# Kernel optimization log

Measured on AMD Instinct MI355X. Metric: run time of the kernel, lower is better.

Reference implementation:

```python
import jax, jax.numpy as jnp
import numpy as np


def setup_inputs() -> dict:
    key = jax.random.key(0)
    B, C, T = 16, 128, 8192
    x = jax.random.normal(key, (B, C, T), dtype=jnp.float32)
    return {"x": x}


def reference(x) -> jnp.ndarray:
    # x: (B, C, T) real EEG signals
    B, C, T = x.shape
    # "Analytic" signal as in the torch code: zero FFT bins >= T//2, then ifft.
    Xf = jnp.fft.fft(x, axis=-1)                       # complex64 (B, C, T)
    keep = (jnp.arange(T) < (T // 2))                  # (T,)
    Xf = jnp.where(keep, Xf, 0.0 + 0.0j)
    xa = jnp.fft.ifft(Xf, axis=-1)                     # complex analytic signal
    phase = jnp.arctan2(xa.imag, xa.real)              # == torch.angle, (B, C, T)

    # PLV_ij = |mean_t exp(i(phase_i - phase_j))|
    # Decompose: Re = mean(cos_i cos_j + sin_i sin_j), Im = mean(sin_i cos_j - cos_i sin_j)
    cos_p = jnp.cos(phase)                             # (B, C, T)
    sin_p = jnp.sin(phase)
    inv_t = jnp.float32(1.0 / T)
    re = (jnp.einsum('bct,bdt->bcd', cos_p, cos_p)
          + jnp.einsum('bct,bdt->bcd', sin_p, sin_p)) * inv_t
    im = (jnp.einsum('bct,bdt->bcd', sin_p, cos_p)
          - jnp.einsum('bct,bdt->bcd', cos_p, sin_p)) * inv_t
    plv = jnp.sqrt(re * re + im * im)                  # (B, C, C)
    return plv
```

## Files before the change

### kernel.cpp

```cpp
#include <hip/hip_runtime.h>
#include <hip/hip_fp16.h>
#include <math.h>

#define T_LEN 8192
#define CHN 128
#define BATCH 16
#define NKCHUNK 16

typedef short bf16x8 __attribute__((ext_vector_type(8)));
typedef float f32x16 __attribute__((ext_vector_type(16)));

#define SIN8 0.3826834323650898f
#define COS8 0.9238795325112868f
#define SROW 72
#define SPLANE (128 * SROW)

__device__ __forceinline__ ushort f2bf(float f) {
    unsigned u = __float_as_uint(f);
    unsigned r = (u + 0x7fffu + ((u >> 16) & 1u)) >> 16;
    return (ushort)r;
}

__device__ __forceinline__ void barrier_lds_only() {
    asm volatile("s_waitcnt lgkmcnt(0)" ::: "memory");
    __builtin_amdgcn_s_barrier();
}

__device__ __forceinline__ float2 cadd(float2 a, float2 b) { return make_float2(a.x + b.x, a.y + b.y); }
__device__ __forceinline__ float2 csub(float2 a, float2 b) { return make_float2(a.x - b.x, a.y - b.y); }
__device__ __forceinline__ float2 cmul(float2 a, float2 b) {
    return make_float2(a.x * b.x - a.y * b.y, a.x * b.y + a.y * b.x);
}

__device__ __forceinline__ void r4f(float2 x0, float2 x1, float2 x2, float2 x3,
                                    float2 wa, float2 wb, float2 wc,
                                    float2& y0, float2& y1, float2& y2, float2& y3) {
    float2 t0 = cadd(x0, x2), t1 = csub(x0, x2);
    float2 t2 = cadd(x1, x3), t3 = csub(x1, x3);
    y0 = cadd(t0, t2);
    y1 = cmul(csub(t0, t2), wb);
    y2 = cmul(make_float2(t1.x + t3.y, t1.y - t3.x), wa);
    y3 = cmul(make_float2(t1.x - t3.y, t1.y + t3.x), wc);
}

__device__ __forceinline__ void r4i(float2 x0, float2 x1, float2 x2, float2 x3,
                                    float2 wa, float2 wb, float2 wc,
                                    float2& y0, float2& y1, float2& y2, float2& y3) {
    float2 a1 = cmul(x1, wb);
    float2 a2 = cmul(x2, wa);
    float2 a3 = cmul(x3, wc);
    float2 u0 = cadd(x0, a1), u1 = csub(x0, a1);
    float2 p = cadd(a2, a3);
    float2 m = make_float2(-(a2.y - a3.y), a2.x - a3.x);
    y0 = cadd(u0, p); y2 = csub(u0, p);
    y1 = cadd(u1, m); y3 = csub(u1, m);
}

__device__ __forceinline__ void r8f(const float2* x, float sn, float cs, float2* y) {
    const float r22 = 0.70710678118654752f;
    float2 w1 = make_float2(cs, sn);
    float2 w2 = make_float2(cs * cs - sn * sn, 2.f * cs * sn);
    float2 w4 = cmul(w2, w2);
    float2 w6 = cmul(w4, w2);
    float2 u0 = cadd(x[0], x[4]), u1 = cadd(x[1], x[5]), u2 = cadd(x[2], x[6]), u3 = cadd(x[3], x[7]);
    float2 e0 = cmul(csub(x[0], x[4]), w1);
    float2 e1 = cmul(csub(x[1], x[5]), w1);
    float2 e2 = cmul(csub(x[2], x[6]), w1);
    float2 e3 = cmul(csub(x[3], x[7]), w1);
    float2 v0 = e0;
    float2 v1 = make_float2(r22 * (e1.x + e1.y), r22 * (e1.y - e1.x));
    float2 v2 = make_float2(e2.y, -e2.x);
    float2 v3 = make_float2(r22 * (e3.y - e3.x), -r22 * (e3.x + e3.y));
    r4f(u0, u1, u2, u3, w2, w4, w6, y[0], y[1], y[2], y[3]);
    r4f(v0, v1, v2, v3, w2, w4, w6, y[4], y[5], y[6], y[7]);
}

__device__ __forceinline__ void r8i(const float2* x, float sn, float cs, float2* y) {
    const float r22 = 0.70710678118654752f;
    float2 w1 = make_float2(cs, sn);
    float2 w2 = make_float2(cs * cs - sn * sn, 2.f * cs * sn);
    float2 w4 = cmul(w2, w2);
    float2 w6 = cmul(w4, w2);
    float2 g0, g1, g2, g3, g4, g5, g6, g7;
    r4i(x[0], x[1], x[2], x[3], w2, w4, w6, g0, g1, g2, g3);
    r4i(x[4], x[5], x[6], x[7], w2, w4, w6, g4, g5, g6, g7);
    float2 t0 = cmul(g4, w1);
    float2 e1 = cmul(g5, w1);
    float2 e2 = cmul(g6, w1);
    float2 e3 = cmul(g7, w1);
    float2 t1 = make_float2(r22 * (e1.x - e1.y), r22 * (e1.x + e1.y));
    float2 t2 = make_float2(-e2.y, e2.x);
    float2 t3 = make_float2(-r22 * (e3.x + e3.y), r22 * (e3.x - e3.y));
    y[0] = cadd(g0, t0); y[4] = csub(g0, t0);
    y[1] = cadd(g1, t1); y[5] = csub(g1, t1);
    y[2] = cadd(g2, t2); y[6] = csub(g2, t2);
    y[3] = cadd(g3, t3); y[7] = csub(g3, t3);
}

__global__ __launch_bounds__(512, 4) void fft_analytic_kernel(const float* __restrict__ x,
                                                              ushort* __restrict__ zc,
                                                              ushort* __restrict__ zs) {
    __shared__ __align__(16) float2 buf[T_LEN];
    const int tid = threadIdx.x;
    const int row = blockIdx.x;
    const float* xr = x + ((size_t)row << 13);

    for (int s = 0; s < 2; ++s) {
        const int g = tid + (s << 9);
        float2 X[8], Y[8];
#pragma unroll
        for (int c = 0; c < 8; ++c) X[c] = make_float2(xr[g + (c << 10)], 0.f);
        float sn, cs;
        __sincosf(-(float)M_PI / 4096.f * (float)g, &sn, &cs);
        r8f(X, sn, cs, Y);
#pragma unroll
        for (int c = 0; c < 8; ++c) buf[g + (c << 10)] = Y[c];
    }
    __syncthreads();

    {
        const float astep = -(float)M_PI / 512.f;
        for (int s = 0; s < 2; ++s) {
            const int g = tid + (s << 9);
            const int j = g & 127;
            const int i = ((g & ~127) << 3) | j;
            float2 xx[8], yy[8];
#pragma unroll
            for (int c = 0; c < 8; ++c) xx[c] = buf[i + c * 128];
            float sn, cs;
            __sincosf(astep * (float)j, &sn, &cs);
            r8f(xx, sn, cs, yy);
#pragma unroll
            for (int c = 0; c < 8; ++c) buf[i + c * 128] = yy[c];
        }
        __syncthreads();
    }

    {
        const float astep = -(float)M_PI / 64.f;
        for (int s = 0; s < 2; ++s) {
            const int g = tid + (s << 9);
            const int j = g & 15;
            const int i = ((g & ~15) << 3) | j;
            float2 xx[8], yy[8];
#pragma unroll
            for (int c = 0; c < 8; ++c) xx[c] = buf[i + c * 16];
            float sn, cs;
            __sincosf(astep * (float)j, &sn, &cs);
            r8f(xx, sn, cs, yy);
#pragma unroll
            for (int c = 0; c < 8; ++c) buf[(i + c * 16) ^ (2 * c)] = yy[c];
        }
        __syncthreads();
    }

    {
        float2 v[16];
        float4* bb = (float4*)buf;
        const int K = tid & 7;
#pragma unroll
        for (int p = 0; p < 8; ++p) {
            float4 f = bb[8 * tid + (p ^ K)];
            v[2 * p]     = make_float2(f.x, f.y);
            v[2 * p + 1] = make_float2(f.z, f.w);
        }
        float2 xe[8], xo[8], E[8], O[8], t[8];
#pragma unroll
        for (int c = 0; c < 8; ++c) { xe[c] = v[2 * c]; xo[c] = v[2 * c + 1]; }
        r8f(xe, 0.f, 1.f, E);
        r8f(xo, -SIN8, COS8, O);
#pragma unroll
        for (int c = 0; c < 8; ++c) t[c] = cadd(E[c], O[c]);
        r8i(t, 0.f, 1.f, xe);
        r8i(t, SIN8, COS8, xo);
#pragma unroll
        for (int p = 0; p < 8; ++p)
            bb[8 * tid + (p ^ K)] = make_float4(xe[p].x, xe[p].y, xo[p].x, xo[p].y);
    }
    __syncthreads();

    {
        const float astep = (float)M_PI / 64.f;
        for (int s = 0; s < 2; ++s) {
            const int g = tid + (s << 9);
            const int j = g & 15;
            const int i = ((g & ~15) << 3) | j;
            float2 xx[8], yy[8];
#pragma unroll
            for (int c = 0; c < 8; ++c) xx[c] = buf[(i + c * 16) ^ (2 * c)];
            float sn, cs;
            __sincosf(astep * (float)j, &sn, &cs);
            r8i(xx, sn, cs, yy);
#pragma unroll
            for (int c = 0; c < 8; ++c) buf[i + c * 16] = yy[c];
        }
        __syncthreads();
    }

    {
        const float astep = (float)M_PI / 512.f;
        for (int s = 0; s < 2; ++s) {
            const int g = tid + (s << 9);
            const int j = g & 127;
            const int i = ((g & ~127) << 3) | j;
            float2 xx[8], yy[8];
#pragma unroll
            for (int c = 0; c < 8; ++c) xx[c] = buf[i + c * 128];
            float sn, cs;
            __sincosf(astep * (float)j, &sn, &cs);
            r8i(xx, sn, cs, yy);
#pragma unroll
            for (int c = 0; c < 8; ++c) buf[i + c * 128] = yy[c];
        }
        __syncthreads();
    }

    ushort* zcr = zc + ((size_t)row << 13);
    ushort* zsr = zs + ((size_t)row << 13);
    for (int s = 0; s < 2; ++s) {
        const int g = tid + (s << 9);
        float2 xx[8], yy[8];
#pragma unroll
        for (int c = 0; c < 8; ++c) xx[c] = buf[g + (c << 10)];
        float sn, cs;
        __sincosf((float)M_PI / 4096.f * (float)g, &sn, &cs);
        r8i(xx, sn, cs, yy);
#pragma unroll
        for (int c = 0; c < 8; ++c) {
            float2 vv = yy[c];
            float n2 = vv.x * vv.x + vv.y * vv.y;
            float cc = 1.f, ss = 0.f;
            if (n2 > 0.f) { float inv = rsqrtf(n2); cc = vv.x * inv; ss = vv.y * inv; }
            zcr[g + (c << 10)] = f2bf(cc);
            zsr[g + (c << 10)] = f2bf(ss);
        }
    }
}

__global__ __launch_bounds__(512, 2) void gram_kernel(const ushort* __restrict__ zc,
                                                      const ushort* __restrict__ zs,
                                                      __half2* __restrict__ partial) {
    const int b = blockIdx.x, kc = blockIdx.y;
    const int tid = threadIdx.x;
    const int wave = tid >> 6;
    const int wr = wave & 3, wcol = wave >> 2;
    const int lane31 = tid & 31;
    const int half = (tid >> 5) & 1;

    __shared__ __align__(16) ushort sZ[2 * SPLANE];

    f32x16 accRe[2], accIm[2];
#pragma unroll
    for (int v = 0; v < 2; ++v)
#pragma unroll
        for (int r = 0; r < 16; ++r) { accRe[v][r] = 0.f; accIm[v][r] = 0.f; }

    const size_t base = ((size_t)b * CHN) << 13;
    const int k0 = kc << 9;

    const ushort* srcs[4];
    int ldst[4];
#pragma unroll
    for (int q = 0; q < 4; ++q) {
        int id = tid + (q << 9);
        int plane = id >> 10;
        int rid = (id >> 3) & 127;
        int ck = id & 7;
        srcs[q] = (plane ? zs : zc) + base + ((size_t)rid << 13) + (size_t)(k0 + ck * 8);
        ldst[q] = plane * SPLANE + rid * SROW + ck * 8;
    }

    uint4 pre[2][4];
#pragma unroll
    for (int q = 0; q < 4; ++q) pre[0][q] = *(const uint4*)srcs[q];
#pragma unroll
    for (int q = 0; q < 4; ++q) pre[1][q] = *(const uint4*)(srcs[q] + 64);

#pragma unroll
    for (int it = 0; it < 8; ++it) {
        barrier_lds_only();
#pragma unroll
        for (int q = 0; q < 4; ++q) *(uint4*)&sZ[ldst[q]] = pre[it & 1][q];
        if (it < 6) {
#pragma unroll
            for (int q = 0; q < 4; ++q)
                pre[it & 1][q] = *(const uint4*)(srcs[q] + (it + 2) * 64);
        }
        barrier_lds_only();
#pragma unroll
        for (int kb = 0; kb < 64; kb += 16) {
            const int aoff = (wr * 32 + lane31) * SROW + kb + half * 8;
            bf16x8 aC = *(const bf16x8*)&sZ[aoff];
            bf16x8 aS = *(const bf16x8*)&sZ[SPLANE + aoff];
            bf16x8 aCn;
#pragma unroll
            for (int r = 0; r < 8; ++r) aCn[r] = (short)(aC[r] ^ (short)0x8000);
            bf16x8 bC[2], bS[2];
#pragma unroll
            for (int v = 0; v < 2; ++v) {
                const int boff = (wcol * 64 + v * 32 + lane31) * SROW + kb + half * 8;
                bC[v] = *(const bf16x8*)&sZ[boff];
                bS[v] = *(const bf16x8*)&sZ[SPLANE + boff];
            }
            accRe[0] = __builtin_amdgcn_mfma_f32_32x32x16_bf16(aC,  bC[0], accRe[0], 0, 0, 0);
            accRe[1] = __builtin_amdgcn_mfma_f32_32x32x16_bf16(aC,  bC[1], accRe[1], 0, 0, 0);
            accIm[0] = __builtin_amdgcn_mfma_f32_32x32x16_bf16(aS,  bC[0], accIm[0], 0, 0, 0);
            accIm[1] = __builtin_amdgcn_mfma_f32_32x32x16_bf16(aS,  bC[1], accIm[1], 0, 0, 0);
            accRe[0] = __builtin_amdgcn_mfma_f32_32x32x16_bf16(aS,  bS[0], accRe[0], 0, 0, 0);
            accRe[1] = __builtin_amdgcn_mfma_f32_32x32x16_bf16(aS,  bS[1], accRe[1], 0, 0, 0);
            accIm[0] = __builtin_amdgcn_mfma_f32_32x32x16_bf16(aCn, bS[0], accIm[0], 0, 0, 0);
            accIm[1] = __builtin_amdgcn_mfma_f32_32x32x16_bf16(aCn, bS[1], accIm[1], 0, 0, 0);
        }
    }

    __half2* pb = partial + ((size_t)(kc * BATCH + b) << 14);
#pragma unroll
    for (int v = 0; v < 2; ++v)
#pragma unroll
        for (int r = 0; r < 16; ++r) {
            int rrow = (r & 3) + 8 * (r >> 2) + 4 * half;
            int i = wr * 32 + rrow;
            int j = wcol * 64 + v * 32 + lane31;
            pb[i * CHN + j] = __floats2half2_rn(accRe[v][r], accIm[v][r]);
        }
}

__global__ __launch_bounds__(256) void reduce_kernel(const __half2* __restrict__ partial,
                                                     float* __restrict__ out) {
    const size_t i = (size_t)blockIdx.x * 256 + threadIdx.x;
    const size_t n = (size_t)BATCH * CHN * CHN;
    if (i >= n) return;
    float re = 0.0f, im = 0.0f;
#pragma unroll
    for (int c = 0; c < NKCHUNK; ++c) {
        float2 p = __half22float2(partial[(size_t)c * n + i]);
        re += p.x;
        im += p.y;
    }
    out[i] = sqrtf(re * re + im * im) * (1.0f / (float)T_LEN);
}

extern "C" void kernel_launch(void* const* d_in, const int* in_sizes, int n_in,
                              void* d_out, int out_size, void* d_ws, size_t ws_size,
                              hipStream_t stream) {
    const float* x = (const float*)d_in[0];
    float* out = (float*)d_out;

    const size_t plane_elems = (size_t)BATCH * CHN * T_LEN;
    ushort* zc = (ushort*)d_ws;
    ushort* zs = zc + plane_elems;
    __half2* partial = (__half2*)((char*)d_ws + 2 * plane_elems * sizeof(ushort));

    fft_analytic_kernel<<<BATCH * CHN, 512, 0, stream>>>(x, zc, zs);

    dim3 g2(BATCH, NKCHUNK);
    gram_kernel<<<g2, 512, 0, stream>>>(zc, zs, partial);

    const int n_out = BATCH * CHN * CHN;
    reduce_kernel<<<(n_out + 255) / 256, 256, 0, stream>>>(partial, out);
}
```

Measured before the change: 177.4 us.

## Precompute FFT twiddles once per thread and split gram kernel across column halves

The FFT kernel now computes each stage's twiddle set once with hardware sin/cos in revolution units and reuses it for the matching inverse stages through conjugate multiplies, instead of calling sincos in every stage. The gram kernel grid gains a column-half dimension, so each block computes a 128x64 tile with one accumulator pair per wave, doubling the number of blocks. This is meant to cut transcendental work and raise occupancy and parallelism in the gram step. The cost is that every block reloads its full A and B slices, so global and LDS traffic rises, and the held twiddles use more registers.

```diff
diff --git a/kernel.cpp b/kernel.cpp
--- a/kernel.cpp
+++ b/kernel.cpp
@@ -12,6 +12,7 @@
 
 #define SIN8 0.3826834323650898f
 #define COS8 0.9238795325112868f
+#define R22  0.70710678118654752f
 #define SROW 72
 #define SPLANE (128 * SROW)
 
@@ -30,6 +31,22 @@
 __device__ __forceinline__ float2 csub(float2 a, float2 b) { return make_float2(a.x - b.x, a.y - b.y); }
 __device__ __forceinline__ float2 cmul(float2 a, float2 b) {
     return make_float2(a.x * b.x - a.y * b.y, a.x * b.y + a.y * b.x);
+}
+__device__ __forceinline__ float2 cmulc(float2 a, float2 b) {
+    return make_float2(a.x * b.x + a.y * b.y, a.y * b.x - a.x * b.y);
+}
+
+struct W8 { float2 w1, w2, w4, w6; };
+
+__device__ __forceinline__ W8 mkw(float rev) {
+    W8 w;
+    float sn = __builtin_amdgcn_sinf(rev);
+    float cs = __builtin_amdgcn_cosf(rev);
+    w.w1 = make_float2(cs, sn);
+    w.w2 = make_float2(cs * cs - sn * sn, 2.f * cs * sn);
+    w.w4 = cmul(w.w2, w.w2);
+    w.w6 = cmul(w.w4, w.w2);
+    return w;
 }
 
 __device__ __forceinline__ void r4f(float2 x0, float2 x1, float2 x2, float2 x3,
@@ -43,12 +60,12 @@
     y3 = cmul(make_float2(t1.x - t3.y, t1.y + t3.x), wc);
 }
 
-__device__ __forceinline__ void r4i(float2 x0, float2 x1, float2 x2, float2 x3,
-                                    float2 wa, float2 wb, float2 wc,
-                                    float2& y0, float2& y1, float2& y2, float2& y3) {
-    float2 a1 = cmul(x1, wb);
-    float2 a2 = cmul(x2, wa);
-    float2 a3 = cmul(x3, wc);
+__device__ __forceinline__ void r4i_c(float2 x0, float2 x1, float2 x2, float2 x3,
+                                      float2 wa, float2 wb, float2 wc,
+                                      float2& y0, float2& y1, float2& y2, float2& y3) {
+    float2 a1 = cmulc(x1, wb);
+    float2 a2 = cmulc(x2, wa);
+    float2 a3 = cmulc(x3, wc);
     float2 u0 = cadd(x0, a1), u1 = csub(x0, a1);
     float2 p = cadd(a2, a3);
     float2 m = make_float2(-(a2.y - a3.y), a2.x - a3.x);
@@ -56,41 +73,31 @@
     y1 = cadd(u1, m); y3 = csub(u1, m);
 }
 
-__device__ __forceinline__ void r8f(const float2* x, float sn, float cs, float2* y) {
-    const float r22 = 0.70710678118654752f;
-    float2 w1 = make_float2(cs, sn);
-    float2 w2 = make_float2(cs * cs - sn * sn, 2.f * cs * sn);
-    float2 w4 = cmul(w2, w2);
-    float2 w6 = cmul(w4, w2);
+__device__ __forceinline__ void r8f_w(const float2* x, W8 w, float2* y) {
     float2 u0 = cadd(x[0], x[4]), u1 = cadd(x[1], x[5]), u2 = cadd(x[2], x[6]), u3 = cadd(x[3], x[7]);
-    float2 e0 = cmul(csub(x[0], x[4]), w1);
-    float2 e1 = cmul(csub(x[1], x[5]), w1);
-    float2 e2 = cmul(csub(x[2], x[6]), w1);
-    float2 e3 = cmul(csub(x[3], x[7]), w1);
+    float2 e0 = cmul(csub(x[0], x[4]), w.w1);
+    float2 e1 = cmul(csub(x[1], x[5]), w.w1);
+    float2 e2 = cmul(csub(x[2], x[6]), w.w1);
+    float2 e3 = cmul(csub(x[3], x[7]), w.w1);
     float2 v0 = e0;
-    float2 v1 = make_float2(r22 * (e1.x + e1.y), r22 * (e1.y - e1.x));
+    float2 v1 = make_float2(R22 * (e1.x + e1.y), R22 * (e1.y - e1.x));
     float2 v2 = make_float2(e2.y, -e2.x);
-    float2 v3 = make_float2(r22 * (e3.y - e3.x), -r22 * (e3.x + e3.y));
-    r4f(u0, u1, u2, u3, w2, w4, w6, y[0], y[1], y[2], y[3]);
-    r4f(v0, v1, v2, v3, w2, w4, w6, y[4], y[5], y[6], y[7]);
-}
-
-__device__ __forceinline__ void r8i(const float2* x, float sn, float cs, float2* y) {
-    const float r22 = 0.70710678118654752f;
-    float2 w1 = make_float2(cs, sn);
-    float2 w2 = make_float2(cs * cs - sn * sn, 2.f * cs * sn);
-    float2 w4 = cmul(w2, w2);
-    float2 w6 = cmul(w4, w2);
+    float2 v3 = make_float2(R22 * (e3.y - e3.x), -R22 * (e3.x + e3.y));
+    r4f(u0, u1, u2, u3, w.w2, w.w4, w.w6, y[0], y[1], y[2], y[3]);
+    r4f(v0, v1, v2, v3, w.w2, w.w4, w.w6, y[4], y[5], y[6], y[7]);
+}
+
+__device__ __forceinline__ void r8i_w(const float2* x, W8 w, float2* y) {
     float2 g0, g1, g2, g3, g4, g5, g6, g7;
-    r4i(x[0], x[1], x[2], x[3], w2, w4, w6, g0, g1, g2, g3);
-    r4i(x[4], x[5], x[6], x[7], w2, w4, w6, g4, g5, g6, g7);
-    float2 t0 = cmul(g4, w1);
-    float2 e1 = cmul(g5, w1);
-    float2 e2 = cmul(g6, w1);
-    float2 e3 = cmul(g7, w1);
-    float2 t1 = make_float2(r22 * (e1.x - e1.y), r22 * (e1.x + e1.y));
+    r4i_c(x[0], x[1], x[2], x[3], w.w2, w.w4, w.w6, g0, g1, g2, g3);
+    r4i_c(x[4], x[5], x[6], x[7], w.w2, w.w4, w.w6, g4, g5, g6, g7);
+    float2 t0 = cmulc(g4, w.w1);
+    float2 e1 = cmulc(g5, w.w1);
+    float2 e2 = cmulc(g6, w.w1);
+    float2 e3 = cmulc(g7, w.w1);
+    float2 t1 = make_float2(R22 * (e1.x - e1.y), R22 * (e1.x + e1.y));
     float2 t2 = make_float2(-e2.y, e2.x);
-    float2 t3 = make_float2(-r22 * (e3.x + e3.y), r22 * (e3.x - e3.y));
+    float2 t3 = make_float2(-R22 * (e3.x + e3.y), R22 * (e3.x - e3.y));
     y[0] = cadd(g0, t0); y[4] = csub(g0, t0);
     y[1] = cadd(g1, t1); y[5] = csub(g1, t1);
     y[2] = cadd(g2, t2); y[6] = csub(g2, t2);
@@ -105,56 +112,54 @@
     const int row = blockIdx.x;
     const float* xr = x + ((size_t)row << 13);
 
+    W8 wL[2];
+    const W8 w128 = mkw((float)(tid & 127) * (-1.f / 1024.f));
+    const W8 w16  = mkw((float)(tid & 15)  * (-1.f / 128.f));
+
+#pragma unroll
     for (int s = 0; s < 2; ++s) {
         const int g = tid + (s << 9);
         float2 X[8], Y[8];
 #pragma unroll
         for (int c = 0; c < 8; ++c) X[c] = make_float2(xr[g + (c << 10)], 0.f);
-        float sn, cs;
-        __sincosf(-(float)M_PI / 4096.f * (float)g, &sn, &cs);
-        r8f(X, sn, cs, Y);
+        wL[s] = mkw((float)g * (-1.f / 8192.f));
+        r8f_w(X, wL[s], Y);
 #pragma unroll
         for (int c = 0; c < 8; ++c) buf[g + (c << 10)] = Y[c];
     }
     __syncthreads();
 
+#pragma unroll
+    for (int s = 0; s < 2; ++s) {
+        const int g = tid + (s << 9);
+        const int i = ((g & ~127) << 3) | (g & 127);
+        float2 xx[8], yy[8];
+#pragma unroll
+        for (int c = 0; c < 8; ++c) xx[c] = buf[i + c * 128];
+        r8f_w(xx, w128, yy);
+#pragma unroll
+        for (int c = 0; c < 8; ++c) buf[i + c * 128] = yy[c];
+    }
+    __syncthreads();
+
+#pragma unroll
+    for (int s = 0; s < 2; ++s) {
+        const int g = tid + (s << 9);
+        const int i = ((g & ~15) << 3) | (g & 15);
+        float2 xx[8], yy[8];
+#pragma unroll
+        for (int c = 0; c < 8; ++c) xx[c] = buf[i + c * 16];
+        r8f_w(xx, w16, yy);
+#pragma unroll
+        for (int c = 0; c < 8; ++c) buf[(i + c * 16) ^ (2 * c)] = yy[c];
+    }
+    __syncthreads();
+
     {
-        const float astep = -(float)M_PI / 512.f;
-        for (int s = 0; s < 2; ++s) {
-            const int g = tid + (s << 9);
-            const int j = g & 127;
-            const int i = ((g & ~127) << 3) | j;
-            float2 xx[8], yy[8];
-#pragma unroll
-            for (int c = 0; c < 8; ++c) xx[c] = buf[i + c * 128];
-            float sn, cs;
-            __sincosf(astep * (float)j, &sn, &cs);
-            r8f(xx, sn, cs, yy);
-#pragma unroll
-            for (int c = 0; c < 8; ++c) buf[i + c * 128] = yy[c];
-        }
-        __syncthreads();
-    }
-
-    {
-        const float astep = -(float)M_PI / 64.f;
-        for (int s = 0; s < 2; ++s) {
-            const int g = tid + (s << 9);
-            const int j = g & 15;
-            const int i = ((g & ~15) << 3) | j;
-            float2 xx[8], yy[8];
-#pragma unroll
-            for (int c = 0; c < 8; ++c) xx[c] = buf[i + c * 16];
-            float sn, cs;
-            __sincosf(astep * (float)j, &sn, &cs);
-            r8f(xx, sn, cs, yy);
-#pragma unroll
-            for (int c = 0; c < 8; ++c) buf[(i + c * 16) ^ (2 * c)] = yy[c];
-        }
-        __syncthreads();
-    }
-
-    {
+        const W8 wID = { make_float2(1.f, 0.f), make_float2(1.f, 0.f),
+                         make_float2(1.f, 0.f), make_float2(1.f, 0.f) };
+        const W8 wO  = { make_float2(COS8, -SIN8), make_float2(R22, -R22),
+                         make_float2(0.f, -1.f),   make_float2(-R22, -R22) };
         float2 v[16];
         float4* bb = (float4*)buf;
         const int K = tid & 7;
@@ -167,64 +172,53 @@
         float2 xe[8], xo[8], E[8], O[8], t[8];
 #pragma unroll
         for (int c = 0; c < 8; ++c) { xe[c] = v[2 * c]; xo[c] = v[2 * c + 1]; }
-        r8f(xe, 0.f, 1.f, E);
-        r8f(xo, -SIN8, COS8, O);
+        r8f_w(xe, wID, E);
+        r8f_w(xo, wO, O);
 #pragma unroll
         for (int c = 0; c < 8; ++c) t[c] = cadd(E[c], O[c]);
-        r8i(t, 0.f, 1.f, xe);
-        r8i(t, SIN8, COS8, xo);
+        r8i_w(t, wID, xe);
+        r8i_w(t, wO, xo);
 #pragma unroll
         for (int p = 0; p < 8; ++p)
             bb[8 * tid + (p ^ K)] = make_float4(xe[p].x, xe[p].y, xo[p].x, xo[p].y);
     }
     __syncthreads();
 
-    {
-        const float astep = (float)M_PI / 64.f;
-        for (int s = 0; s < 2; ++s) {
-            const int g = tid + (s << 9);
-            const int j = g & 15;
-            const int i = ((g & ~15) << 3) | j;
-            float2 xx[8], yy[8];
-#pragma unroll
-            for (int c = 0; c < 8; ++c) xx[c] = buf[(i + c * 16) ^ (2 * c)];
-            float sn, cs;
-            __sincosf(astep * (float)j, &sn, &cs);
-            r8i(xx, sn, cs, yy);
-#pragma unroll
-            for (int c = 0; c < 8; ++c) buf[i + c * 16] = yy[c];
-        }
-        __syncthreads();
-    }
-
-    {
-        const float astep = (float)M_PI / 512.f;
-        for (int s = 0; s < 2; ++s) {
-            const int g = tid + (s << 9);
-            const int j = g & 127;
-            const int i = ((g & ~127) << 3) | j;
-            float2 xx[8], yy[8];
-#pragma unroll
-            for (int c = 0; c < 8; ++c) xx[c] = buf[i + c * 128];
-            float sn, cs;
-            __sincosf(astep * (float)j, &sn, &cs);
-            r8i(xx, sn, cs, yy);
-#pragma unroll
-            for (int c = 0; c < 8; ++c) buf[i + c * 128] = yy[c];
-        }
-        __syncthreads();
-    }
+#pragma unroll
+    for (int s = 0; s < 2; ++s) {
+        const int g = tid + (s << 9);
+        const int i = ((g & ~15) << 3) | (g & 15);
+        float2 xx[8], yy[8];
+#pragma unroll
+        for (int c = 0; c < 8; ++c) xx[c] = buf[(i + c * 16) ^ (2 * c)];
+        r8i_w(xx, w16, yy);
+#pragma unroll
+        for (int c = 0; c < 8; ++c) buf[i + c * 16] = yy[c];
+    }
+    __syncthreads();
+
+#pragma unroll
+    for (int s = 0; s < 2; ++s) {
+        const int g = tid + (s << 9);
+        const int i = ((g & ~127) << 3) | (g & 127);
+        float2 xx[8], yy[8];
+#pragma unroll
+        for (int c = 0; c < 8; ++c) xx[c] = buf[i + c * 128];
+        r8i_w(xx, w128, yy);
+#pragma unroll
+        for (int c = 0; c < 8; ++c) buf[i + c * 128] = yy[c];
+    }
+    __syncthreads();
 
     ushort* zcr = zc + ((size_t)row << 13);
     ushort* zsr = zs + ((size_t)row << 13);
+#pragma unroll
     for (int s = 0; s < 2; ++s) {
         const int g = tid + (s << 9);
         float2 xx[8], yy[8];
 #pragma unroll
         for (int c = 0; c < 8; ++c) xx[c] = buf[g + (c << 10)];
-        float sn, cs;
-        __sincosf((float)M_PI / 4096.f * (float)g, &sn, &cs);
-        r8i(xx, sn, cs, yy);
+        r8i_w(xx, wL[s], yy);
 #pragma unroll
         for (int c = 0; c < 8; ++c) {
             float2 vv = yy[c];
@@ -240,20 +234,19 @@
 __global__ __launch_bounds__(512, 2) void gram_kernel(const ushort* __restrict__ zc,
                                                       const ushort* __restrict__ zs,
                                                       __half2* __restrict__ partial) {
-    const int b = blockIdx.x, kc = blockIdx.y;
+    const int b = blockIdx.x, jh = blockIdx.y, kc = blockIdx.z;
+    const int j0 = jh * 64;
     const int tid = threadIdx.x;
     const int wave = tid >> 6;
-    const int wr = wave & 3, wcol = wave >> 2;
+    const int wr = wave & 3, wc2 = wave >> 2;
     const int lane31 = tid & 31;
     const int half = (tid >> 5) & 1;
 
     __shared__ __align__(16) ushort sZ[2 * SPLANE];
 
-    f32x16 accRe[2], accIm[2];
-#pragma unroll
-    for (int v = 0; v < 2; ++v)
-#pragma unroll
-        for (int r = 0; r < 16; ++r) { accRe[v][r] = 0.f; accIm[v][r] = 0.f; }
+    f32x16 accRe, accIm;
+#pragma unroll
+    for (int r = 0; r < 16; ++r) { accRe[r] = 0.f; accIm[r] = 0.f; }
 
     const size_t base = ((size_t)b * CHN) << 13;
     const int k0 = kc << 9;
@@ -295,34 +288,24 @@
             bf16x8 aCn;
 #pragma unroll
             for (int r = 0; r < 8; ++r) aCn[r] = (short)(aC[r] ^ (short)0x8000);
-            bf16x8 bC[2], bS[2];
-#pragma unroll
-            for (int v = 0; v < 2; ++v) {
-                const int boff = (wcol * 64 + v * 32 + lane31) * SROW + kb + half * 8;
-                bC[v] = *(const bf16x8*)&sZ[boff];
-                bS[v] = *(const bf16x8*)&sZ[SPLANE + boff];
-            }
-            accRe[0] = __builtin_amdgcn_mfma_f32_32x32x16_bf16(aC,  bC[0], accRe[0], 0, 0, 0);
-            accRe[1] = __builtin_amdgcn_mfma_f32_32x32x16_bf16(aC,  bC[1], accRe[1], 0, 0, 0);
-            accIm[0] = __builtin_amdgcn_mfma_f32_32x32x16_bf16(aS,  bC[0], accIm[0], 0, 0, 0);
-            accIm[1] = __builtin_amdgcn_mfma_f32_32x32x16_bf16(aS,  bC[1], accIm[1], 0, 0, 0);
-            accRe[0] = __builtin_amdgcn_mfma_f32_32x32x16_bf16(aS,  bS[0], accRe[0], 0, 0, 0);
-            accRe[1] = __builtin_amdgcn_mfma_f32_32x32x16_bf16(aS,  bS[1], accRe[1], 0, 0, 0);
-            accIm[0] = __builtin_amdgcn_mfma_f32_32x32x16_bf16(aCn, bS[0], accIm[0], 0, 0, 0);
-            accIm[1] = __builtin_amdgcn_mfma_f32_32x32x16_bf16(aCn, bS[1], accIm[1], 0, 0, 0);
+            const int boff = (j0 + wc2 * 32 + lane31) * SROW + kb + half * 8;
+            bf16x8 bC = *(const bf16x8*)&sZ[boff];
+            bf16x8 bS = *(const bf16x8*)&sZ[SPLANE + boff];
+            accRe = __builtin_amdgcn_mfma_f32_32x32x16_bf16(aC,  bC, accRe, 0, 0, 0);
+            accIm = __builtin_amdgcn_mfma_f32_32x32x16_bf16(aS,  bC, accIm, 0, 0, 0);
+            accRe = __builtin_amdgcn_mfma_f32_32x32x16_bf16(aS,  bS, accRe, 0, 0, 0);
+            accIm = __builtin_amdgcn_mfma_f32_32x32x16_bf16(aCn, bS, accIm, 0, 0, 0);
         }
     }
 
     __half2* pb = partial + ((size_t)(kc * BATCH + b) << 14);
 #pragma unroll
-    for (int v = 0; v < 2; ++v)
-#pragma unroll
-        for (int r = 0; r < 16; ++r) {
-            int rrow = (r & 3) + 8 * (r >> 2) + 4 * half;
-            int i = wr * 32 + rrow;
-            int j = wcol * 64 + v * 32 + lane31;
-            pb[i * CHN + j] = __floats2half2_rn(accRe[v][r], accIm[v][r]);
-        }
+    for (int r = 0; r < 16; ++r) {
+        int rrow = (r & 3) + 8 * (r >> 2) + 4 * half;
+        int i = wr * 32 + rrow;
+        int j = j0 + wc2 * 32 + lane31;
+        pb[i * CHN + j] = __floats2half2_rn(accRe[r], accIm[r]);
+    }
 }
 
 __global__ __launch_bounds__(256) void reduce_kernel(const __half2* __restrict__ partial,
@@ -353,7 +336,7 @@
 
     fft_analytic_kernel<<<BATCH * CHN, 512, 0, stream>>>(x, zc, zs);
 
-    dim3 g2(BATCH, NKCHUNK);
+    dim3 g2(BATCH, 2, NKCHUNK);
     gram_kernel<<<g2, 512, 0, stream>>>(zc, zs, partial);
 
     const int n_out = BATCH * CHN * CHN;
```

New measurement: 242.9 us. 1.37x slower.
